# Kernel tuning notes

Measured on AMD Instinct MI355X. Metric: run time of the kernel, lower is better.

Reference implementation:

```python
import jax, jax.numpy as jnp
import numpy as np

DELTA_SCALE = 0.99
DELTA_MIN = 0.01


def setup_inputs() -> dict:
    key = jax.random.key(0)
    ks = jax.random.split(key, 6)
    B, S, Dm, N = 8, 4096, 1024, 16
    x = jax.random.normal(ks[0], (B, S, Dm), dtype=jnp.float32)
    A = jax.random.normal(ks[1], (N,), dtype=jnp.float32) * 0.1 - 1.0
    W_b = jax.random.normal(ks[2], (N, Dm), dtype=jnp.float32) / np.sqrt(Dm)
    b_b = jnp.zeros((N,), dtype=jnp.float32)
    W_c = jax.random.normal(ks[3], (Dm, N), dtype=jnp.float32) / np.sqrt(N)
    b_c = jnp.zeros((Dm,), dtype=jnp.float32)
    D = jnp.ones((Dm,), dtype=jnp.float32)
    W_t = jax.random.normal(ks[4], (1, Dm), dtype=jnp.float32) / np.sqrt(Dm)
    b_t = jnp.zeros((1,), dtype=jnp.float32)
    W_o = jax.random.normal(ks[5], (Dm, Dm), dtype=jnp.float32) / np.sqrt(Dm)
    b_o = jnp.zeros((Dm,), dtype=jnp.float32)
    return {"x": x, "A": A, "W_b": W_b, "b_b": b_b, "W_c": W_c, "b_c": b_c,
            "D": D, "W_t": W_t, "b_t": b_t, "W_o": W_o, "b_o": b_o}


def _scan_combine(left, right):
    # h_t = a_t * h_{t-1} + b_t ; compose two affine maps
    a_l, u_l = left
    a_r, u_r = right
    return (a_l * a_r, a_r * u_l + u_r)


def reference(x, A, W_b, b_b, W_c, b_c, D, W_t, b_t, W_o, b_o):
    # x: [B, S, Dm]
    delta = jax.nn.sigmoid(jnp.einsum('bsd,od->bso', x, W_t) + b_t)  # [B,S,1]
    delta = delta * DELTA_SCALE + DELTA_MIN
    Bu = jnp.einsum('bsd,nd->bsn', x, W_b) + b_b                     # [B,S,N]
    A_exp = jnp.exp(A[None, None, :] * delta)                        # [B,S,N]
    # Parallel associative scan over time: h_t = A_exp_t * h_{t-1} + Bu_t
    _, h = jax.lax.associative_scan(_scan_combine, (A_exp, Bu), axis=1)
    outputs = jnp.einsum('bsn,dn->bsd', h, W_c) + b_c                # [B,S,Dm]
    y = outputs + x * D[None, None, :]
    y = jnp.einsum('bsd,od->bso', y, W_o) + b_o                      # dropout = eval identity
    return y
```

## Files before the change

kernel.cpp:

```cpp
#include <hip/hip_runtime.h>
#include <hip/hip_bf16.h>
#include <cstdint>
#include <cstddef>

#define B_SZ 8
#define S_SZ 4096
#define DM   1024
#define NS   16
#define M_SZ (B_SZ * S_SZ)

typedef __attribute__((ext_vector_type(4))) float f32x4;
typedef __attribute__((ext_vector_type(8))) short short8;
typedef __attribute__((ext_vector_type(4))) unsigned short ushort4v;
typedef __attribute__((ext_vector_type(8))) unsigned short ushort8v;

__device__ __forceinline__ unsigned short f2bf(float f) {
  unsigned u = __float_as_uint(f);
  u += 0x7fffu + ((u >> 16) & 1u);
  return (unsigned short)(u >> 16);
}

__device__ __forceinline__ short8 cvt8(f32x4 a, f32x4 b) {
  short8 r;
  r[0] = (short)f2bf(a[0]); r[1] = (short)f2bf(a[1]);
  r[2] = (short)f2bf(a[2]); r[3] = (short)f2bf(a[3]);
  r[4] = (short)f2bf(b[0]); r[5] = (short)f2bf(b[1]);
  r[6] = (short)f2bf(b[2]); r[7] = (short)f2bf(b[3]);
  return r;
}

__device__ __forceinline__ void gl_lds16(const void* g, void* l) {
  __builtin_amdgcn_global_load_lds(
      (const __attribute__((address_space(1))) void*)g,
      (__attribute__((address_space(3))) void*)l, 16, 0, 0);
}

#define SB() __builtin_amdgcn_sched_barrier(0)
__device__ __forceinline__ void bar() { SB(); __builtin_amdgcn_s_barrier(); SB(); }
#define VMW4 asm volatile("s_waitcnt vmcnt(4)" ::: "memory")
#define VMW0 asm volatile("s_waitcnt vmcnt(0)" ::: "memory")
#define VMNOP (void)0

__global__ __launch_bounds__(256) void k0_prep(
    const float* __restrict__ Wo, const float* __restrict__ D,
    const float* __restrict__ Wc, const float* __restrict__ bc,
    const float* __restrict__ bo, unsigned short* __restrict__ WoD16,
    unsigned short* __restrict__ Wco16, float* __restrict__ bz,
    const float* __restrict__ Wb, const float* __restrict__ Wt,
    unsigned short* __restrict__ W16s) {
  const int t = threadIdx.x;
  if (blockIdx.x >= 1024) {
    const int col = blockIdx.x - 1024;
    f32x4 a = {0.f, 0.f, 0.f, 0.f};
    if (col < 16)       a = *(const f32x4*)(Wb + (size_t)col * DM + t * 4);
    else if (col == 16) a = *(const f32x4*)(Wt + t * 4);
    ushort4v u;
#pragma unroll
    for (int i = 0; i < 4; ++i) u[i] = f2bf(a[i]);
    *(ushort4v*)((char*)W16s + ((col * 2048 + t * 8) ^ ((col & 7) << 4))) = u;
    return;
  }
  const int o = blockIdx.x;
  const float* wor = Wo + (size_t)o * DM;

  f32x4 wv = *(const f32x4*)(wor + t * 4);
  f32x4 dv = *(const f32x4*)(D + t * 4);
  ushort4v u;
#pragma unroll
  for (int i = 0; i < 4; ++i) u[i] = f2bf(wv[i] * dv[i]);
  *(ushort4v*)(WoD16 + (size_t)o * DM + t * 4) = u;

  const int n = t & 15, ds = t >> 4;
  float s = 0.f;
  const float* wod = wor + ds * 64;
  const float* wcd = Wc + (size_t)(ds * 64) * NS + n;
#pragma unroll 8
  for (int j = 0; j < 64; ++j) s += wod[j] * wcd[j * NS];

  f32x4 bcv = *(const f32x4*)(bc + t * 4);
  float pb = wv[0] * bcv[0] + wv[1] * bcv[1] + wv[2] * bcv[2] + wv[3] * bcv[3];

  __shared__ float red[16][17];
  __shared__ float redb[256];
  red[n][ds] = s;
  redb[t] = pb;
  __syncthreads();
  if (t < 16) {
    float acc = 0.f;
#pragma unroll
    for (int k = 0; k < 16; ++k) acc += red[t][k];
    Wco16[(size_t)o * 32 + t] = f2bf(acc);
    Wco16[(size_t)o * 32 + 16 + t] = 0;
  }
  if (t < 64) {
    float s4 = redb[t] + redb[t + 64] + redb[t + 128] + redb[t + 192];
#pragma unroll
    for (int mb = 1; mb < 64; mb <<= 1) s4 += __shfl_xor(s4, mb, 64);
    if (t == 0) bz[o] = bo[o] + s4;
  }
}

__global__ __launch_bounds__(256) void k1_proj(
    const float* __restrict__ x, const float* __restrict__ A,
    const unsigned short* __restrict__ W16s,
    const float* __restrict__ bb, const float* __restrict__ bt,
    float* __restrict__ Ae, float* __restrict__ Bu,
    unsigned short* __restrict__ x16) {
  __shared__ __align__(16) char Wlds[65536];
  __shared__ float Bu_s[16][65];
  __shared__ float z_s[64];
  const int tid = threadIdx.x, lane = tid & 63, w = tid >> 6;
  const int p = lane & 15, g = lane >> 4;

#pragma unroll
  for (int i = 0; i < 16; ++i)
    gl_lds16((const char*)W16s + (w * 16 + i) * 1024 + lane * 16,
             Wlds + (w * 16 + i) * 1024);
  __syncthreads();

  const int m0 = blockIdx.x * 64;
  const int m = m0 + w * 16 + p;
  const float* xp = x + (size_t)m * DM;
  unsigned short* xo = x16 + (size_t)m * DM;
  f32x4 acc0 = {0.f, 0.f, 0.f, 0.f}, acc1 = {0.f, 0.f, 0.f, 0.f};
  const int cb0 = p * 2048;
  const int cb1 = (16 + p) * 2048;
  const int sw0 = (p & 7) << 4;

#pragma unroll 2
  for (int kk = 0; kk < 32; ++kk) {
    const int k0 = kk * 32 + g * 8;
    f32x4 xa = *(const f32x4*)(xp + k0);
    f32x4 xb = *(const f32x4*)(xp + k0 + 4);
    short8 af = cvt8(xa, xb);
    *(short8*)(xo + k0) = af;
    const int kb = kk * 64 + g * 16;
    short8 b0 = *(const short8*)(Wlds + ((cb0 + kb) ^ sw0));
    short8 b1 = *(const short8*)(Wlds + ((cb1 + kb) ^ sw0));
    acc0 = __builtin_amdgcn_mfma_f32_16x16x32_bf16(af, b0, acc0, 0, 0, 0);
    acc1 = __builtin_amdgcn_mfma_f32_16x16x32_bf16(af, b1, acc1, 0, 0, 0);
  }

  const float bbn = bb[p];
#pragma unroll
  for (int r = 0; r < 4; ++r) Bu_s[p][w * 16 + g * 4 + r] = acc0[r] + bbn;
  if (p == 0) {
#pragma unroll
    for (int r = 0; r < 4; ++r) z_s[w * 16 + g * 4 + r] = acc1[r];
  }
  __syncthreads();

  const int b_idx = m0 >> 12;
  const int s0 = m0 & (S_SZ - 1);
  const int n = tid >> 4, j0 = (tid & 15) * 4;
  const float an = A[n];
  const float bt0 = bt[0];
  size_t off = ((size_t)(b_idx * NS + n)) * S_SZ + s0 + j0;
#pragma unroll
  for (int jj = 0; jj < 4; ++jj) {
    float z = z_s[j0 + jj] + bt0;
    float delta = 1.f / (1.f + __expf(-z));
    delta = delta * 0.99f + 0.01f;
    Ae[off + jj] = __expf(an * delta);
    Bu[off + jj] = Bu_s[n][j0 + jj];
  }
}

__global__ __launch_bounds__(256) void k2a(float* __restrict__ Ae, float* __restrict__ Bu,
                                           float* __restrict__ agg_a, float* __restrict__ agg_u) {
  const int l = threadIdx.x & 63, w = threadIdx.x >> 6;
  const int cid = blockIdx.x * 4 + w;
  float* ap = Ae + (size_t)cid * 256;
  float* up = Bu + (size_t)cid * 256;
  float ca = 1.f, cu = 0.f;
#pragma unroll 1
  for (int seg = 0; seg < 4; ++seg) {
    float a = ap[seg * 64 + l], u = up[seg * 64 + l];
#pragma unroll
    for (int off = 1; off < 64; off <<= 1) {
      float aL = __shfl_up(a, off, 64);
      float uL = __shfl_up(u, off, 64);
      if (l >= off) { u = a * uL + u; a = aL * a; }
    }
    float At = ca * a, Ut = a * cu + u;
    ap[seg * 64 + l] = At;
    up[seg * 64 + l] = Ut;
    ca = __shfl(At, 63, 64);
    cu = __shfl(Ut, 63, 64);
  }
  if (l == 0) { agg_a[cid] = ca; agg_u[cid] = cu; }
}

__global__ __launch_bounds__(256) void k2c(const float* __restrict__ Ae,
                                           const float* __restrict__ Bu,
                                           const float* __restrict__ agg_a,
                                           const float* __restrict__ agg_u,
                                           unsigned short* __restrict__ h16) {
  const int t = threadIdx.x;
  const int m = blockIdx.x * 256 + t;
  const int b = m >> 12, s = m & 4095, c = s >> 8;
  __shared__ float cp_s[16];
  if (t < 16) {
    float cu = 0.f;
    const int base = (b * 16 + t) * 16;
    for (int c2 = 0; c2 < c; ++c2) cu = agg_a[base + c2] * cu + agg_u[base + c2];
    cp_s[t] = cu;
  }
  __syncthreads();
  unsigned short o[32];
#pragma unroll
  for (int n = 0; n < 16; ++n) {
    size_t idx = ((size_t)(b * 16 + n)) * 4096 + s;
    float h = Ae[idx] * cp_s[n] + Bu[idx];
    o[n] = f2bf(h);
  }
#pragma unroll
  for (int n = 16; n < 32; ++n) o[n] = 0;
  unsigned short* dst = h16 + (size_t)m * 32;
#pragma unroll
  for (int q = 0; q < 4; ++q) *(ushort8v*)(dst + q * 8) = *(const ushort8v*)(o + q * 8);
}

__global__ __launch_bounds__(512, 2) void k4_gemm(
    const unsigned short* __restrict__ x16, const unsigned short* __restrict__ h16,
    const unsigned short* __restrict__ WoD16, const unsigned short* __restrict__ Wco16,
    const float* __restrict__ bz, float* __restrict__ C) {
  __shared__ __align__(16) char smem[131072];
  const int tid = threadIdx.x;
  const int swzid = (blockIdx.x & 7) * 64 + (blockIdx.x >> 3);
  const int by = swzid >> 2;
  const int bx = swzid & 3;
  const int lane = tid & 63;
  const int w = tid >> 6;
  const int wm = w >> 2, wn = w & 3;
  const int p = lane & 15, g = lane >> 4;
  const int cbsw = (g * 16) ^ (((p >> 1) & 3) << 4);

  f32x4 acc[8][4];
#pragma unroll
  for (int i = 0; i < 8; ++i)
#pragma unroll
    for (int j = 0; j < 4; ++j) acc[i][j] = (f32x4){0.f, 0.f, 0.f, 0.f};

  {
    short8 ah[8], bh[4];
#pragma unroll
    for (int mi = 0; mi < 8; ++mi)
      ah[mi] = *(const short8*)(h16 + (size_t)(by * 256 + wm * 128 + mi * 16 + p) * 32 + g * 8);
#pragma unroll
    for (int ni = 0; ni < 4; ++ni)
      bh[ni] = *(const short8*)(Wco16 + (size_t)(bx * 256 + wn * 64 + ni * 16 + p) * 32 + g * 8);
#pragma unroll
    for (int mi = 0; mi < 8; ++mi)
#pragma unroll
      for (int ni = 0; ni < 4; ++ni)
        acc[mi][ni] = __builtin_amdgcn_mfma_f32_16x16x32_bf16(ah[mi], bh[ni],
                                                              acc[mi][ni], 0, 0, 0);
  }
  SB();

  const char* Ag = (const char*)(x16 + (size_t)(by * 256) * DM);
  const char* Bg = (const char*)(WoD16 + (size_t)(bx * 256) * DM);
  const int L0 = tid * 16, L1 = 8192 + tid * 16;
  const int r0 = L0 >> 6, r1 = L1 >> 6;
  const size_t ga0 = (size_t)r0 * 2048 + ((L0 & 63) ^ (((r0 >> 1) & 3) << 4));
  const size_t ga1 = (size_t)r1 * 2048 + ((L1 & 63) ^ (((r1 >> 1) & 3) << 4));

#define STG_A(d, kh, t_)                                                        \
  do { const int ko_ = (t_) * 128 + (kh) * 64;                                  \
    gl_lds16(Ag + ga0 + ko_, smem + (d) * 32768 + (kh) * 16384 + L0);           \
    gl_lds16(Ag + ga1 + ko_, smem + (d) * 32768 + (kh) * 16384 + L1); } while (0)
#define STG_B(d, kh, t_)                                                        \
  do { const int ko_ = (t_) * 128 + (kh) * 64;                                  \
    gl_lds16(Bg + ga0 + ko_, smem + 65536 + (d) * 32768 + (kh) * 16384 + L0);   \
    gl_lds16(Bg + ga1 + ko_, smem + 65536 + (d) * 32768 + (kh) * 16384 + L1); } while (0)

#define PHASE(d, kh, mh, STAGE_STMT, VMSTMT)                                    \
  do {                                                                          \
    const char* ab_ = smem + (d) * 32768 + (kh) * 16384;                        \
    const char* bb_ = smem + 65536 + (d) * 32768 + (kh) * 16384;                \
    short8 af0 = *(const short8*)(ab_ + (wm * 128 + ((mh) * 4 + 0) * 16 + p) * 64 + cbsw); \
    short8 af1 = *(const short8*)(ab_ + (wm * 128 + ((mh) * 4 + 1) * 16 + p) * 64 + cbsw); \
    short8 af2 = *(const short8*)(ab_ + (wm * 128 + ((mh) * 4 + 2) * 16 + p) * 64 + cbsw); \
    short8 af3 = *(const short8*)(ab_ + (wm * 128 + ((mh) * 4 + 3) * 16 + p) * 64 + cbsw); \
    short8 bf0 = *(const short8*)(bb_ + (wn * 64 + 0 * 16 + p) * 64 + cbsw);    \
    short8 bf1 = *(const short8*)(bb_ + (wn * 64 + 1 * 16 + p) * 64 + cbsw);    \
    short8 bf2 = *(const short8*)(bb_ + (wn * 64 + 2 * 16 + p) * 64 + cbsw);    \
    short8 bf3 = *(const short8*)(bb_ + (wn * 64 + 3 * 16 + p) * 64 + cbsw);    \
    STAGE_STMT;                                                                 \
    bar();                                                                      \
    __builtin_amdgcn_s_setprio(1);                                              \
    acc[(mh)*4+0][0] = __builtin_amdgcn_mfma_f32_16x16x32_bf16(af0, bf0, acc[(mh)*4+0][0], 0, 0, 0); \
    acc[(mh)*4+0][1] = __builtin_amdgcn_mfma_f32_16x16x32_bf16(af0, bf1, acc[(mh)*4+0][1], 0, 0, 0); \
    acc[(mh)*4+0][2] = __builtin_amdgcn_mfma_f32_16x16x32_bf16(af0, bf2, acc[(mh)*4+0][2], 0, 0, 0); \
    acc[(mh)*4+0][3] = __builtin_amdgcn_mfma_f32_16x16x32_bf16(af0, bf3, acc[(mh)*4+0][3], 0, 0, 0); \
    acc[(mh)*4+1][0] = __builtin_amdgcn_mfma_f32_16x16x32_bf16(af1, bf0, acc[(mh)*4+1][0], 0, 0, 0); \
    acc[(mh)*4+1][1] = __builtin_amdgcn_mfma_f32_16x16x32_bf16(af1, bf1, acc[(mh)*4+1][1], 0, 0, 0); \
    acc[(mh)*4+1][2] = __builtin_amdgcn_mfma_f32_16x16x32_bf16(af1, bf2, acc[(mh)*4+1][2], 0, 0, 0); \
    acc[(mh)*4+1][3] = __builtin_amdgcn_mfma_f32_16x16x32_bf16(af1, bf3, acc[(mh)*4+1][3], 0, 0, 0); \
    acc[(mh)*4+2][0] = __builtin_amdgcn_mfma_f32_16x16x32_bf16(af2, bf0, acc[(mh)*4+2][0], 0, 0, 0); \
    acc[(mh)*4+2][1] = __builtin_amdgcn_mfma_f32_16x16x32_bf16(af2, bf1, acc[(mh)*4+2][1], 0, 0, 0); \
    acc[(mh)*4+2][2] = __builtin_amdgcn_mfma_f32_16x16x32_bf16(af2, bf2, acc[(mh)*4+2][2], 0, 0, 0); \
    acc[(mh)*4+2][3] = __builtin_amdgcn_mfma_f32_16x16x32_bf16(af2, bf3, acc[(mh)*4+2][3], 0, 0, 0); \
    acc[(mh)*4+3][0] = __builtin_amdgcn_mfma_f32_16x16x32_bf16(af3, bf0, acc[(mh)*4+3][0], 0, 0, 0); \
    acc[(mh)*4+3][1] = __builtin_amdgcn_mfma_f32_16x16x32_bf16(af3, bf1, acc[(mh)*4+3][1], 0, 0, 0); \
    acc[(mh)*4+3][2] = __builtin_amdgcn_mfma_f32_16x16x32_bf16(af3, bf2, acc[(mh)*4+3][2], 0, 0, 0); \
    acc[(mh)*4+3][3] = __builtin_amdgcn_mfma_f32_16x16x32_bf16(af3, bf3, acc[(mh)*4+3][3], 0, 0, 0); \
    __builtin_amdgcn_s_setprio(0);                                              \
    VMSTMT;                                                                     \
    bar();                                                                      \
  } while (0)

  STG_A(0, 0, 0); STG_B(0, 0, 0); STG_A(0, 1, 0); STG_B(0, 1, 0);
  STG_A(1, 0, 1); STG_B(1, 0, 1);
  VMW4;
  bar();

#pragma unroll 1
  for (int i = 0; i < 8; ++i) {
    const int t1 = 2 * i + 1;
    const int t2 = (2 * i + 2 > 15) ? 15 : 2 * i + 2;
    const int t3 = (2 * i + 3 > 15) ? 15 : 2 * i + 3;
    PHASE(0, 0, 0, STG_A(1, 1, t1), VMNOP);
    PHASE(0, 0, 1, STG_B(1, 1, t1), VMNOP);
    PHASE(0, 1, 0, STG_A(0, 0, t2), VMNOP);
    PHASE(0, 1, 1, STG_B(0, 0, t2), VMW4);
    PHASE(1, 0, 0, STG_A(0, 1, t2), VMNOP);
    PHASE(1, 0, 1, STG_B(0, 1, t2), VMNOP);
    PHASE(1, 1, 0, STG_A(1, 0, t3), VMNOP);
    PHASE(1, 1, 1, STG_B(1, 0, t3), VMW4);
  }
  VMW0;
#undef PHASE
#undef STG_A
#undef STG_B

#pragma unroll
  for (int ni = 0; ni < 4; ++ni) {
    const int c0 = bx * 256 + wn * 64 + ni * 16 + p;
    const float bzv = bz[c0];
#pragma unroll
    for (int mi = 0; mi < 8; ++mi) {
      const int r0w = by * 256 + wm * 128 + mi * 16 + g * 4;
#pragma unroll
      for (int r = 0; r < 4; ++r)
        C[(size_t)(r0w + r) * DM + c0] = acc[mi][ni][r] + bzv;
    }
  }
}

extern "C" void kernel_launch(void* const* d_in, const int* in_sizes, int n_in,
                              void* d_out, int out_size, void* d_ws, size_t ws_size,
                              hipStream_t stream) {
  const float* x  = (const float*)d_in[0];
  const float* A  = (const float*)d_in[1];
  const float* Wb = (const float*)d_in[2];
  const float* bb = (const float*)d_in[3];
  const float* Wc = (const float*)d_in[4];
  const float* bc = (const float*)d_in[5];
  const float* D  = (const float*)d_in[6];
  const float* Wt = (const float*)d_in[7];
  const float* bt = (const float*)d_in[8];
  const float* Wo = (const float*)d_in[9];
  const float* bo = (const float*)d_in[10];
  float* out = (float*)d_out;

  char* ws = (char*)d_ws;
  float* Ae            = (float*)(ws);
  float* Bu            = (float*)(ws + (2u << 20));
  unsigned short* h16  = (unsigned short*)(ws + (4u << 20));
  unsigned short* WoD16= (unsigned short*)(ws + (6u << 20));
  unsigned short* Wco16= (unsigned short*)(ws + (8u << 20));
  float* bz            = (float*)(ws + (8u << 20) + (64u << 10));
  unsigned short* W16s = (unsigned short*)(ws + (8u << 20) + (68u << 10));
  float* agg_a         = (float*)(ws + (8u << 20) + (132u << 10));
  float* agg_u         = (float*)(ws + (8u << 20) + (140u << 10));
  unsigned short* x16  = (unsigned short*)(ws + (9u << 20));

  k0_prep<<<1056, 256, 0, stream>>>(Wo, D, Wc, bc, bo, WoD16, Wco16, bz, Wb, Wt, W16s);
  k1_proj<<<512, 256, 0, stream>>>(x, A, W16s, bb, bt, Ae, Bu, x16);
  k2a<<<512, 256, 0, stream>>>(Ae, Bu, agg_a, agg_u);
  k2c<<<128, 256, 0, stream>>>(Ae, Bu, agg_a, agg_u, h16);
  k4_gemm<<<512, 512, 0, stream>>>(x16, h16, WoD16, Wco16, bz, out);
}
```

Before: 356.0 us.

## Restructure GEMM main loop into 4-stage ring with register-double-buffered fragments

The main k4_gemm loop changes from a 2-buffer, half-K phase schedule to a 4-slot LDS ring of 32-wide K chunks. The fragments for the next chunk are prefetched into a second register set while the MFMAs run on the current set, and each phase has one barrier instead of two. This is meant to hide LDS read latency behind MFMA work and to cut barrier overhead. It also changes the k2c launch shape to 256 blocks of 128 threads and raises the k1_proj loop unroll from 2 to 4. The register-double-buffered fragments raise VGPR pressure, which could reduce occupancy.

```diff
diff --git a/kernel.cpp b/kernel.cpp
--- a/kernel.cpp
+++ b/kernel.cpp
@@ -39,7 +39,6 @@
 __device__ __forceinline__ void bar() { SB(); __builtin_amdgcn_s_barrier(); SB(); }
 #define VMW4 asm volatile("s_waitcnt vmcnt(4)" ::: "memory")
 #define VMW0 asm volatile("s_waitcnt vmcnt(0)" ::: "memory")
-#define VMNOP (void)0
 
 __global__ __launch_bounds__(256) void k0_prep(
     const float* __restrict__ Wo, const float* __restrict__ D,
@@ -127,7 +126,7 @@
   const int cb1 = (16 + p) * 2048;
   const int sw0 = (p & 7) << 4;
 
-#pragma unroll 2
+#pragma unroll 4
   for (int kk = 0; kk < 32; ++kk) {
     const int k0 = kk * 32 + g * 8;
     f32x4 xa = *(const f32x4*)(xp + k0);
@@ -191,13 +190,13 @@
   if (l == 0) { agg_a[cid] = ca; agg_u[cid] = cu; }
 }
 
-__global__ __launch_bounds__(256) void k2c(const float* __restrict__ Ae,
+__global__ __launch_bounds__(128) void k2c(const float* __restrict__ Ae,
                                            const float* __restrict__ Bu,
                                            const float* __restrict__ agg_a,
                                            const float* __restrict__ agg_u,
                                            unsigned short* __restrict__ h16) {
   const int t = threadIdx.x;
-  const int m = blockIdx.x * 256 + t;
+  const int m = blockIdx.x * 128 + t;
   const int b = m >> 12, s = m & 4095, c = s >> 8;
   __shared__ float cp_s[16];
   if (t < 16) {
@@ -266,74 +265,79 @@
   const size_t ga0 = (size_t)r0 * 2048 + ((L0 & 63) ^ (((r0 >> 1) & 3) << 4));
   const size_t ga1 = (size_t)r1 * 2048 + ((L1 & 63) ^ (((r1 >> 1) & 3) << 4));
 
-#define STG_A(d, kh, t_)                                                        \
-  do { const int ko_ = (t_) * 128 + (kh) * 64;                                  \
-    gl_lds16(Ag + ga0 + ko_, smem + (d) * 32768 + (kh) * 16384 + L0);           \
-    gl_lds16(Ag + ga1 + ko_, smem + (d) * 32768 + (kh) * 16384 + L1); } while (0)
-#define STG_B(d, kh, t_)                                                        \
-  do { const int ko_ = (t_) * 128 + (kh) * 64;                                  \
-    gl_lds16(Bg + ga0 + ko_, smem + 65536 + (d) * 32768 + (kh) * 16384 + L0);   \
-    gl_lds16(Bg + ga1 + ko_, smem + 65536 + (d) * 32768 + (kh) * 16384 + L1); } while (0)
-
-#define PHASE(d, kh, mh, STAGE_STMT, VMSTMT)                                    \
-  do {                                                                          \
-    const char* ab_ = smem + (d) * 32768 + (kh) * 16384;                        \
-    const char* bb_ = smem + 65536 + (d) * 32768 + (kh) * 16384;                \
-    short8 af0 = *(const short8*)(ab_ + (wm * 128 + ((mh) * 4 + 0) * 16 + p) * 64 + cbsw); \
-    short8 af1 = *(const short8*)(ab_ + (wm * 128 + ((mh) * 4 + 1) * 16 + p) * 64 + cbsw); \
-    short8 af2 = *(const short8*)(ab_ + (wm * 128 + ((mh) * 4 + 2) * 16 + p) * 64 + cbsw); \
-    short8 af3 = *(const short8*)(ab_ + (wm * 128 + ((mh) * 4 + 3) * 16 + p) * 64 + cbsw); \
-    short8 bf0 = *(const short8*)(bb_ + (wn * 64 + 0 * 16 + p) * 64 + cbsw);    \
-    short8 bf1 = *(const short8*)(bb_ + (wn * 64 + 1 * 16 + p) * 64 + cbsw);    \
-    short8 bf2 = *(const short8*)(bb_ + (wn * 64 + 2 * 16 + p) * 64 + cbsw);    \
-    short8 bf3 = *(const short8*)(bb_ + (wn * 64 + 3 * 16 + p) * 64 + cbsw);    \
-    STAGE_STMT;                                                                 \
-    bar();                                                                      \
-    __builtin_amdgcn_s_setprio(1);                                              \
-    acc[(mh)*4+0][0] = __builtin_amdgcn_mfma_f32_16x16x32_bf16(af0, bf0, acc[(mh)*4+0][0], 0, 0, 0); \
-    acc[(mh)*4+0][1] = __builtin_amdgcn_mfma_f32_16x16x32_bf16(af0, bf1, acc[(mh)*4+0][1], 0, 0, 0); \
-    acc[(mh)*4+0][2] = __builtin_amdgcn_mfma_f32_16x16x32_bf16(af0, bf2, acc[(mh)*4+0][2], 0, 0, 0); \
-    acc[(mh)*4+0][3] = __builtin_amdgcn_mfma_f32_16x16x32_bf16(af0, bf3, acc[(mh)*4+0][3], 0, 0, 0); \
-    acc[(mh)*4+1][0] = __builtin_amdgcn_mfma_f32_16x16x32_bf16(af1, bf0, acc[(mh)*4+1][0], 0, 0, 0); \
-    acc[(mh)*4+1][1] = __builtin_amdgcn_mfma_f32_16x16x32_bf16(af1, bf1, acc[(mh)*4+1][1], 0, 0, 0); \
-    acc[(mh)*4+1][2] = __builtin_amdgcn_mfma_f32_16x16x32_bf16(af1, bf2, acc[(mh)*4+1][2], 0, 0, 0); \
-    acc[(mh)*4+1][3] = __builtin_amdgcn_mfma_f32_16x16x32_bf16(af1, bf3, acc[(mh)*4+1][3], 0, 0, 0); \
-    acc[(mh)*4+2][0] = __builtin_amdgcn_mfma_f32_16x16x32_bf16(af2, bf0, acc[(mh)*4+2][0], 0, 0, 0); \
-    acc[(mh)*4+2][1] = __builtin_amdgcn_mfma_f32_16x16x32_bf16(af2, bf1, acc[(mh)*4+2][1], 0, 0, 0); \
-    acc[(mh)*4+2][2] = __builtin_amdgcn_mfma_f32_16x16x32_bf16(af2, bf2, acc[(mh)*4+2][2], 0, 0, 0); \
-    acc[(mh)*4+2][3] = __builtin_amdgcn_mfma_f32_16x16x32_bf16(af2, bf3, acc[(mh)*4+2][3], 0, 0, 0); \
-    acc[(mh)*4+3][0] = __builtin_amdgcn_mfma_f32_16x16x32_bf16(af3, bf0, acc[(mh)*4+3][0], 0, 0, 0); \
-    acc[(mh)*4+3][1] = __builtin_amdgcn_mfma_f32_16x16x32_bf16(af3, bf1, acc[(mh)*4+3][1], 0, 0, 0); \
-    acc[(mh)*4+3][2] = __builtin_amdgcn_mfma_f32_16x16x32_bf16(af3, bf2, acc[(mh)*4+3][2], 0, 0, 0); \
-    acc[(mh)*4+3][3] = __builtin_amdgcn_mfma_f32_16x16x32_bf16(af3, bf3, acc[(mh)*4+3][3], 0, 0, 0); \
-    __builtin_amdgcn_s_setprio(0);                                              \
-    VMSTMT;                                                                     \
-    bar();                                                                      \
+#define STG(r_, c_)                                                            \
+  do { const int ko_ = (c_) * 64;                                              \
+    gl_lds16(Ag + ga0 + ko_, smem + (r_) * 16384 + L0);                        \
+    gl_lds16(Ag + ga1 + ko_, smem + (r_) * 16384 + L1);                        \
+    gl_lds16(Bg + ga0 + ko_, smem + 65536 + (r_) * 16384 + L0);                \
+    gl_lds16(Bg + ga1 + ko_, smem + 65536 + (r_) * 16384 + L1); } while (0)
+
+  short8 fA[2][8];
+  short8 fB[2][4];
+
+#define LOADFRAG(S, RG)                                                        \
+  do {                                                                         \
+    const char* ar_ = smem + (RG) * 16384 + (wm * 128 + p) * 64 + cbsw;        \
+    const char* br_ = smem + 65536 + (RG) * 16384 + (wn * 64 + p) * 64 + cbsw; \
+    fA[S][0] = *(const short8*)(ar_ + 0 * 1024);                               \
+    fA[S][1] = *(const short8*)(ar_ + 1 * 1024);                               \
+    fA[S][2] = *(const short8*)(ar_ + 2 * 1024);                               \
+    fA[S][3] = *(const short8*)(ar_ + 3 * 1024);                               \
+    fA[S][4] = *(const short8*)(ar_ + 4 * 1024);                               \
+    fA[S][5] = *(const short8*)(ar_ + 5 * 1024);                               \
+    fA[S][6] = *(const short8*)(ar_ + 6 * 1024);                               \
+    fA[S][7] = *(const short8*)(ar_ + 7 * 1024);                               \
+    fB[S][0] = *(const short8*)(br_ + 0 * 1024);                               \
+    fB[S][1] = *(const short8*)(br_ + 1 * 1024);                               \
+    fB[S][2] = *(const short8*)(br_ + 2 * 1024);                               \
+    fB[S][3] = *(const short8*)(br_ + 3 * 1024);                               \
   } while (0)
 
-  STG_A(0, 0, 0); STG_B(0, 0, 0); STG_A(0, 1, 0); STG_B(0, 1, 0);
-  STG_A(1, 0, 1); STG_B(1, 0, 1);
+#define MM1(S, MI)                                                                            \
+  acc[MI][0] = __builtin_amdgcn_mfma_f32_16x16x32_bf16(fA[S][MI], fB[S][0], acc[MI][0], 0, 0, 0); \
+  acc[MI][1] = __builtin_amdgcn_mfma_f32_16x16x32_bf16(fA[S][MI], fB[S][1], acc[MI][1], 0, 0, 0); \
+  acc[MI][2] = __builtin_amdgcn_mfma_f32_16x16x32_bf16(fA[S][MI], fB[S][2], acc[MI][2], 0, 0, 0); \
+  acc[MI][3] = __builtin_amdgcn_mfma_f32_16x16x32_bf16(fA[S][MI], fB[S][3], acc[MI][3], 0, 0, 0);
+
+#define MM(S)                                                                  \
+  do { __builtin_amdgcn_s_setprio(1);                                          \
+    MM1(S, 0) MM1(S, 1) MM1(S, 2) MM1(S, 3)                                    \
+    MM1(S, 4) MM1(S, 5) MM1(S, 6) MM1(S, 7)                                    \
+    __builtin_amdgcn_s_setprio(0); } while (0)
+
+#define PHASE(J, S, c3)                                                        \
+  do {                                                                         \
+    LOADFRAG(1 - (S), ((J) + 1) & 3);                                          \
+    STG(((J) + 3) & 3, c3);                                                    \
+    SB();                                                                      \
+    MM(S);                                                                     \
+    VMW4;                                                                      \
+    bar();                                                                     \
+  } while (0)
+
+  STG(0, 0); STG(1, 1); STG(2, 2);
   VMW4;
   bar();
+  LOADFRAG(0, 0);
 
 #pragma unroll 1
-  for (int i = 0; i < 8; ++i) {
-    const int t1 = 2 * i + 1;
-    const int t2 = (2 * i + 2 > 15) ? 15 : 2 * i + 2;
-    const int t3 = (2 * i + 3 > 15) ? 15 : 2 * i + 3;
-    PHASE(0, 0, 0, STG_A(1, 1, t1), VMNOP);
-    PHASE(0, 0, 1, STG_B(1, 1, t1), VMNOP);
-    PHASE(0, 1, 0, STG_A(0, 0, t2), VMNOP);
-    PHASE(0, 1, 1, STG_B(0, 0, t2), VMW4);
-    PHASE(1, 0, 0, STG_A(0, 1, t2), VMNOP);
-    PHASE(1, 0, 1, STG_B(0, 1, t2), VMNOP);
-    PHASE(1, 1, 0, STG_A(1, 0, t3), VMNOP);
-    PHASE(1, 1, 1, STG_B(1, 0, t3), VMW4);
+  for (int it = 0; it < 8; ++it) {
+    const int c0_ = it * 4;
+    const int t0 = (c0_ + 3 > 31) ? 31 : c0_ + 3;
+    const int t1 = (c0_ + 4 > 31) ? 31 : c0_ + 4;
+    const int t2 = (c0_ + 5 > 31) ? 31 : c0_ + 5;
+    const int t3 = (c0_ + 6 > 31) ? 31 : c0_ + 6;
+    PHASE(0, 0, t0);
+    PHASE(1, 1, t1);
+    PHASE(2, 0, t2);
+    PHASE(3, 1, t3);
   }
   VMW0;
 #undef PHASE
-#undef STG_A
-#undef STG_B
+#undef MM
+#undef MM1
+#undef LOADFRAG
+#undef STG
 
 #pragma unroll
   for (int ni = 0; ni < 4; ++ni) {
@@ -380,6 +384,6 @@
   k0_prep<<<1056, 256, 0, stream>>>(Wo, D, Wc, bc, bo, WoD16, Wco16, bz, Wb, Wt, W16s);
   k1_proj<<<512, 256, 0, stream>>>(x, A, W16s, bb, bt, Ae, Bu, x16);
   k2a<<<512, 256, 0, stream>>>(Ae, Bu, agg_a, agg_u);
-  k2c<<<128, 256, 0, stream>>>(Ae, Bu, agg_a, agg_u, h16);
+  k2c<<<256, 128, 0, stream>>>(Ae, Bu, agg_a, agg_u, h16);
   k4_gemm<<<512, 512, 0, stream>>>(x16, h16, WoD16, Wco16, bz, out);
 }
```

Result: faster. 342.3 us (-3.9%).
